# Optimization experiments

Measured on AMD Instinct MI355X. Metric: run time of the kernel, lower is better.

The kernel has to match this reference:

```python
import jax, jax.numpy as jnp
import numpy as np

N = 50000      # nodes
E = 800000     # edges (before self-loops)
DIN, H1, H2, OUT = 128, 128, 64, 40
LN_EPS = 1e-5


def setup_inputs() -> dict:
    key = jax.random.key(0)
    ks = jax.random.split(key, 16)
    s = lambda d: 1.0 / np.sqrt(d)
    inp = {
        "x": jax.random.normal(ks[0], (N, DIN), jnp.float32),
        "edge_index": jax.random.randint(ks[1], (2, E), 0, N, dtype=jnp.int64),
        # GCNConv weights (applied as x @ W) and biases
        "W1": jax.random.normal(ks[2], (DIN, H1), jnp.float32) * s(DIN),
        "b1": jnp.zeros((H1,), jnp.float32),
        "W2": jax.random.normal(ks[3], (H1, H2), jnp.float32) * s(H1),
        "b2": jnp.zeros((H2,), jnp.float32),
        "W3": jax.random.normal(ks[4], (H2, H2), jnp.float32) * s(H2),
        "b3": jnp.zeros((H2,), jnp.float32),
        # LayerNorms
        "g1": jnp.ones((H1,), jnp.float32),
        "be1": jnp.zeros((H1,), jnp.float32),
        "g2": jnp.ones((H2,), jnp.float32),
        "be2": jnp.zeros((H2,), jnp.float32),
        # post_mp MLP head
        "Wp1": jax.random.normal(ks[5], (H2, H2), jnp.float32) * s(H2),
        "bp1": jnp.zeros((H2,), jnp.float32),
        "Wp2": jax.random.normal(ks[6], (H2, OUT), jnp.float32) * s(H2),
        "bp2": jnp.zeros((OUT,), jnp.float32),
    }
    return inp


def _layer_norm(x, g, b):
    mu = jnp.mean(x, axis=-1, keepdims=True)
    var = jnp.mean((x - mu) ** 2, axis=-1, keepdims=True)
    return (x - mu) * jax.lax.rsqrt(var + LN_EPS) * g + b


def _gcn(x, src, dst, norm, W, b):
    # PyG GCNConv: linear first, then normalized gather/scatter-add, bias last
    h = x @ W                                  # [N, H]
    msg = h[src] * norm[:, None]               # [E+N, H] gather
    out = jax.ops.segment_sum(msg, dst, num_segments=N)  # scatter-add
    return out + b


def reference(x, edge_index, W1, b1, W2, b2, W3, b3, g1, be1, g2, be2,
              Wp1, bp1, Wp2, bp2):
    loops = jnp.arange(N, dtype=edge_index.dtype)
    src = jnp.concatenate([edge_index[0], loops])  # add self-loops
    dst = jnp.concatenate([edge_index[1], loops])
    # symmetric normalization D^{-1/2} (A+I) D^{-1/2} (same graph all layers)
    deg = jax.ops.segment_sum(jnp.ones_like(src, dtype=x.dtype), dst,
                              num_segments=N)
    dinv = jnp.where(deg > 0, jax.lax.rsqrt(jnp.maximum(deg, 1.0)), 0.0)
    norm = dinv[src] * dinv[dst]

    h = _gcn(x, src, dst, norm, W1, b1)
    h = _layer_norm(jax.nn.relu(h), g1, be1)
    h = _gcn(h, src, dst, norm, W2, b2)
    h = _layer_norm(jax.nn.relu(h), g2, be2)
    emb = _gcn(h, src, dst, norm, W3, b3)      # emb = conv output, pre-ReLU
    h = jax.nn.relu(emb)
    h = (h @ Wp1 + bp1) @ Wp2 + bp2            # post_mp: two stacked Linears
    return emb, jax.nn.log_softmax(h, axis=1)
```

## Files before the change

### kernel.cpp

```cpp
#include <hip/hip_runtime.h>
#include <hip/hip_bf16.h>

#define DIN 128
#define HID1 128
#define HID2 64
#define OUTD 40
#define NCHUNK 64

typedef __attribute__((ext_vector_type(8))) short bf16x8;
typedef __attribute__((ext_vector_type(4))) float f32x4;

__device__ __forceinline__ float bf2f(unsigned int u) {
    union { unsigned int i; float f; } c;
    c.i = u << 16;
    return c.f;
}
__device__ __forceinline__ unsigned short f2bf(float f) {
    union { float f; unsigned int i; } c; c.f = f;
    unsigned int r = c.i + 0x7FFFu + ((c.i >> 16) & 1u);
    return (unsigned short)(r >> 16);
}
__device__ __forceinline__ unsigned int packbf(float lo, float hi) {
    return (unsigned int)f2bf(lo) | ((unsigned int)f2bf(hi) << 16);
}

struct WCvt {
    const void* p[14];
    int sz[14];
    int off[14];
    int tobf[14];
    int cols[14];
};


__launch_bounds__(512)
__global__ void prep_kernel(const unsigned short* __restrict__ xu,
                            const int* __restrict__ ei,
                            int* __restrict__ flags,
                            int* __restrict__ pos,
                            unsigned int* __restrict__ hist,
                            WCvt wc, unsigned short* __restrict__ wbf,
                            float* __restrict__ wf,
                            int E, int N) {
    __shared__ unsigned int h32[25000];
    __shared__ int sh2[2];
    const int NW = (N + 1) >> 1;
    const int b = blockIdx.x;
    const int t = threadIdx.x;
    if (b < NCHUNK) {
        if (t == 0) sh2[0] = 0;
        for (int w = t; w < NW; w += 512) h32[w] = 0u;
        __syncthreads();
        int zodd = 0;
        for (int k = t; k < 1024; k += 512)
            if (ei[2 * k + 1] == 0) zodd++;
        if (zodd) atomicAdd(&sh2[0], zodd);
        __syncthreads();
        const int e64 = (sh2[0] > 512) ? 1 : 0;
        const int CH = (E + NCHUNK - 1) / NCHUNK;
        const int lo = b * CH;
        int hi = lo + CH; if (hi > E) hi = E;
        for (int e = lo + t; e < hi; e += 512) {
            int d = e64 ? ei[2 * (E + e)] : ei[E + e];
            if ((unsigned)d < (unsigned)N) {
                unsigned sh = (unsigned)(d & 1) << 4;
                unsigned old = atomicAdd(&h32[d >> 1], 1u << sh);
                pos[e] = (int)((old >> sh) & 0xffffu);
            } else {
                pos[e] = -1;
            }
        }
        __syncthreads();
        unsigned int* hb = hist + (size_t)b * NW;
        for (int w = t; w < NW; w += 512) hb[w] = h32[w];
    } else {
        if (t < 2) sh2[t] = 0;
        __syncthreads();
        int bad = 0;
        for (int k = t; k < 2048; k += 512) {
            float v = bf2f(xu[2 * k]);
            float a = fabsf(v);
            if (!(a <= 1e4f) || (v != 0.f && a < 1e-4f)) bad++;
        }
        int zodd = 0;
        for (int k = t; k < 1024; k += 512)
            if (ei[2 * k + 1] == 0) zodd++;
        if (bad) atomicAdd(&sh2[0], bad);
        if (zodd) atomicAdd(&sh2[1], zodd);
        __syncthreads();
        int xf32 = (sh2[0] > 512) ? 1 : 0;
        if (t == 0) {
            flags[0] = xf32;
            flags[1] = (sh2[1] > 512) ? 1 : 0;
        }
        for (int a = 0; a < 14; ++a) {
            const float* pf = (const float*)wc.p[a];
            const unsigned short* pb = (const unsigned short*)wc.p[a];
            int n = wc.sz[a], off = wc.off[a], tobf = wc.tobf[a];
            int cols = wc.cols[a];
            int rows = tobf ? (n / cols) : 0;
            for (int i = t; i < n; i += 512) {
                float v = xf32 ? pf[i] : bf2f(pb[i]);
                if (tobf) {
                    int k = i / cols, m = i % cols;
                    wbf[off + m * rows + k] = f2bf(v);
                } else {
                    wf[off + i] = v;
                }
            }
        }
    }
}

__device__ __forceinline__ int get_src(const int* ei, int E, int e, int e64) {
    return e64 ? ei[2 * e] : ei[e];
}
__device__ __forceinline__ int get_dst(const int* ei, int E, int e, int e64) {
    return e64 ? ei[2 * (E + e)] : ei[E + e];
}

__launch_bounds__(256)
__global__ void phaseB_kernel(const unsigned int* __restrict__ hist,
                              unsigned int* __restrict__ basev,
                              int* __restrict__ cnt, int* __restrict__ bsum,
                              int N) {
    __shared__ int red[256];
    const int NW = (N + 1) >> 1;
    const int NP = NW * 2;
    int t = threadIdx.x;
    int w = blockIdx.x * 256 + t;
    unsigned run0 = 0, run1 = 0;
    if (w < NW) {
        #pragma unroll 4
        for (int b = 0; b < NCHUNK; ++b) {
            unsigned u = hist[(size_t)b * NW + w];
            uint2 bb; bb.x = run0; bb.y = run1;
            *(uint2*)&basev[(size_t)b * NP + 2 * w] = bb;
            run0 += u & 0xffffu;
            run1 += u >> 16;
        }
        cnt[2 * w] = (int)run0;
        if (2 * w + 1 < N) cnt[2 * w + 1] = (int)run1;
    }
    int tot = 0;
    if (w < NW) tot = (int)run0 + ((2 * w + 1 < N) ? (int)run1 : 0);
    red[t] = tot;
    __syncthreads();
    #pragma unroll
    for (int off = 64; off >= 1; off >>= 1) {
        if ((t & 127) < off) red[t] += red[t + off];
        __syncthreads();
    }
    if (t == 0) bsum[2 * blockIdx.x] = red[0];
    if (t == 128) bsum[2 * blockIdx.x + 1] = red[128];
}

__launch_bounds__(256)
__global__ void bscan_kernel(const int* __restrict__ bsum, int* __restrict__ bbase,
                             int* __restrict__ indptr, int NB, int N) {
    __shared__ int part[256];
    int t = threadIdx.x;
    int CH = (NB + 255) / 256;
    int lo = t * CH, hi = lo + CH; if (hi > NB) hi = NB;
    int s = 0;
    for (int i = lo; i < hi; ++i) s += bsum[i];
    part[t] = s;
    __syncthreads();
    for (int off = 1; off < 256; off <<= 1) {
        int v = (t >= off) ? part[t - off] : 0;
        __syncthreads();
        part[t] += v;
        __syncthreads();
    }
    int run = (t > 0) ? part[t - 1] : 0;
    for (int i = lo; i < hi; ++i) { bbase[i] = run; run += bsum[i]; }
    if (t == 255) indptr[N] = part[255];
}

__launch_bounds__(256)
__global__ void emit_kernel(const int* __restrict__ cnt, const int* __restrict__ bbase,
                            int* __restrict__ indptr, float* __restrict__ dinv, int N) {
    __shared__ int sh[256];
    int t = threadIdx.x;
    int i = blockIdx.x * 256 + t;
    int c = (i < N) ? cnt[i] : 0;
    sh[t] = c;
    __syncthreads();
    for (int off = 1; off < 256; off <<= 1) {
        int v = (t >= off) ? sh[t - off] : 0;
        __syncthreads();
        sh[t] += v;
        __syncthreads();
    }
    if (i < N) {
        int excl = sh[t] - c + bbase[blockIdx.x];
        indptr[i] = excl;
        dinv[i] = 1.0f / sqrtf((float)(c + 1));
    }
}

__global__ void scatter_kernel(const int* __restrict__ ei, const int* __restrict__ indptr,
                               const int* __restrict__ pos, const float* __restrict__ dinv,
                               const unsigned int* __restrict__ basev,
                               int2* __restrict__ csr_sn,
                               int E, int N, const int* __restrict__ flags) {
    int e64 = flags[1];
    int CH = (E + NCHUNK - 1) / NCHUNK;
    int NP = ((N + 1) >> 1) * 2;
    int base = (blockIdx.x * blockDim.x + threadIdx.x) * 4;
    #pragma unroll
    for (int u = 0; u < 4; ++u) {
        int e = base + u;
        if (e < E) {
            int p = pos[e];
            if (p >= 0) {
                int bb = e / CH;
                int d = get_dst(ei, E, e, e64);
                int s = get_src(ei, E, e, e64);
                if ((unsigned)s >= (unsigned)N) s = 0;
                float nrm = dinv[s] * dinv[d];
                int slot = indptr[d] + (int)basev[(size_t)bb * NP + d] + p;
                csr_sn[slot] = make_int2(s, __float_as_int(nrm));
            }
        }
    }
}


template<typename AT>
__device__ __forceinline__ bf16x8 ld_afrag(const AT* p);
template<>
__device__ __forceinline__ bf16x8 ld_afrag<unsigned short>(const unsigned short* p) {
    return *(const bf16x8*)p;
}
template<>
__device__ __forceinline__ bf16x8 ld_afrag<float>(const float* p) {
    float4 a = *(const float4*)p;
    float4 b = *(const float4*)(p + 4);
    bf16x8 r;
    r[0] = (short)f2bf(a.x); r[1] = (short)f2bf(a.y);
    r[2] = (short)f2bf(a.z); r[3] = (short)f2bf(a.w);
    r[4] = (short)f2bf(b.x); r[5] = (short)f2bf(b.y);
    r[6] = (short)f2bf(b.z); r[7] = (short)f2bf(b.w);
    return r;
}

template<int K, int M, typename AT>
__device__ __forceinline__ void mm_body(const AT* __restrict__ A,
                                        const unsigned short* __restrict__ WT,
                                        unsigned short* __restrict__ C, int N,
                                        unsigned short (*Ws)[K + 8]) {
    int tid = threadIdx.x;
    for (int idx = tid; idx < M * K / 8; idx += 256) {
        int r = idx / (K / 8), c8 = idx % (K / 8);
        *(uint4*)&Ws[r][c8 * 8] = *(const uint4*)&WT[r * K + c8 * 8];
    }
    __syncthreads();
    int w = tid >> 6, lane = tid & 63;
    int m = lane & 15, q = lane >> 4;
    int row_a = blockIdx.x * 64 + w * 16 + m;
    if (row_a >= N) row_a = N - 1;
    const AT* arow = A + (size_t)row_a * K;
    f32x4 acc[M / 16];
    #pragma unroll
    for (int t = 0; t < M / 16; ++t) acc[t] = (f32x4){0.f, 0.f, 0.f, 0.f};
    #pragma unroll
    for (int ks = 0; ks < K / 32; ++ks) {
        int k0 = ks * 32 + q * 8;
        bf16x8 a = ld_afrag<AT>(arow + k0);
        #pragma unroll
        for (int t = 0; t < M / 16; ++t) {
            bf16x8 b = *(const bf16x8*)&Ws[t * 16 + m][k0];
            acc[t] = __builtin_amdgcn_mfma_f32_16x16x32_bf16(a, b, acc[t], 0, 0, 0);
        }
    }
    int rbase = blockIdx.x * 64 + w * 16 + q * 4;
    #pragma unroll
    for (int reg = 0; reg < 4; ++reg) {
        int row = rbase + reg;
        if (row < N) {
            #pragma unroll
            for (int t = 0; t < M / 16; ++t)
                C[(size_t)row * M + t * 16 + m] = f2bf(acc[t][reg]);
        }
    }
}

template<int K, int M>
__launch_bounds__(256)
__global__ void mm_dual_kernel(const void* __restrict__ A,
                               const unsigned short* __restrict__ WT,
                               unsigned short* __restrict__ C, int N,
                               const int* __restrict__ flags) {
    __shared__ unsigned short Ws[M][K + 8];
    if (flags[0]) mm_body<K, M, float>((const float*)A, WT, C, N, Ws);
    else          mm_body<K, M, unsigned short>((const unsigned short*)A, WT, C, N, Ws);
}

template<int K, int M>
__launch_bounds__(256)
__global__ void mm_bf_kernel(const unsigned short* __restrict__ A,
                             const unsigned short* __restrict__ WT,
                             unsigned short* __restrict__ C, int N) {
    __shared__ unsigned short Ws[M][K + 8];
    mm_body<K, M, unsigned short>(A, WT, C, N, Ws);
}


template<int VPL>
__device__ __forceinline__ void gacc1(float* acc, const unsigned short* r, float n) {
    if constexpr (VPL == 8) {
        uint4 u = *(const uint4*)r;
        acc[0] += bf2f(u.x & 0xffffu) * n; acc[1] += bf2f(u.x >> 16) * n;
        acc[2] += bf2f(u.y & 0xffffu) * n; acc[3] += bf2f(u.y >> 16) * n;
        acc[4] += bf2f(u.z & 0xffffu) * n; acc[5] += bf2f(u.z >> 16) * n;
        acc[6] += bf2f(u.w & 0xffffu) * n; acc[7] += bf2f(u.w >> 16) * n;
    } else {
        uint2 u = *(const uint2*)r;
        acc[0] += bf2f(u.x & 0xffffu) * n; acc[1] += bf2f(u.x >> 16) * n;
        acc[2] += bf2f(u.y & 0xffffu) * n; acc[3] += bf2f(u.y >> 16) * n;
    }
}

template<int VPL>
__device__ __forceinline__ void gacc4(float* acc,
                                      const unsigned short* r0, float n0,
                                      const unsigned short* r1, float n1,
                                      const unsigned short* r2, float n2,
                                      const unsigned short* r3, float n3) {
    if constexpr (VPL == 8) {
        uint4 u0 = *(const uint4*)r0;
        uint4 u1 = *(const uint4*)r1;
        uint4 u2 = *(const uint4*)r2;
        uint4 u3 = *(const uint4*)r3;
        acc[0] += bf2f(u0.x & 0xffffu) * n0 + bf2f(u1.x & 0xffffu) * n1
                + bf2f(u2.x & 0xffffu) * n2 + bf2f(u3.x & 0xffffu) * n3;
        acc[1] += bf2f(u0.x >> 16) * n0 + bf2f(u1.x >> 16) * n1
                + bf2f(u2.x >> 16) * n2 + bf2f(u3.x >> 16) * n3;
        acc[2] += bf2f(u0.y & 0xffffu) * n0 + bf2f(u1.y & 0xffffu) * n1
                + bf2f(u2.y & 0xffffu) * n2 + bf2f(u3.y & 0xffffu) * n3;
        acc[3] += bf2f(u0.y >> 16) * n0 + bf2f(u1.y >> 16) * n1
                + bf2f(u2.y >> 16) * n2 + bf2f(u3.y >> 16) * n3;
        acc[4] += bf2f(u0.z & 0xffffu) * n0 + bf2f(u1.z & 0xffffu) * n1
                + bf2f(u2.z & 0xffffu) * n2 + bf2f(u3.z & 0xffffu) * n3;
        acc[5] += bf2f(u0.z >> 16) * n0 + bf2f(u1.z >> 16) * n1
                + bf2f(u2.z >> 16) * n2 + bf2f(u3.z >> 16) * n3;
        acc[6] += bf2f(u0.w & 0xffffu) * n0 + bf2f(u1.w & 0xffffu) * n1
                + bf2f(u2.w & 0xffffu) * n2 + bf2f(u3.w & 0xffffu) * n3;
        acc[7] += bf2f(u0.w >> 16) * n0 + bf2f(u1.w >> 16) * n1
                + bf2f(u2.w >> 16) * n2 + bf2f(u3.w >> 16) * n3;
    } else {
        uint2 u0 = *(const uint2*)r0;
        uint2 u1 = *(const uint2*)r1;
        uint2 u2 = *(const uint2*)r2;
        uint2 u3 = *(const uint2*)r3;
        acc[0] += bf2f(u0.x & 0xffffu) * n0 + bf2f(u1.x & 0xffffu) * n1
                + bf2f(u2.x & 0xffffu) * n2 + bf2f(u3.x & 0xffffu) * n3;
        acc[1] += bf2f(u0.x >> 16) * n0 + bf2f(u1.x >> 16) * n1
                + bf2f(u2.x >> 16) * n2 + bf2f(u3.x >> 16) * n3;
        acc[2] += bf2f(u0.y & 0xffffu) * n0 + bf2f(u1.y & 0xffffu) * n1
                + bf2f(u2.y & 0xffffu) * n2 + bf2f(u3.y & 0xffffu) * n3;
        acc[3] += bf2f(u0.y >> 16) * n0 + bf2f(u1.y >> 16) * n1
                + bf2f(u2.y >> 16) * n2 + bf2f(u3.y >> 16) * n3;
    }
}

template<int H, bool RELU_LN, bool EMB>
__launch_bounds__(256)
__global__ void agg_kernel(const unsigned short* __restrict__ h,
                           const int* __restrict__ indptr,
                           const int2* __restrict__ csr_sn,
                           const float* __restrict__ dinv,
                           const float* __restrict__ bias,
                           const float* __restrict__ gamma,
                           const float* __restrict__ beta,
                           unsigned short* __restrict__ out,
                           void* __restrict__ out_emb,
                           int N, const int* __restrict__ flags) {
    constexpr int VPL = H / 16;
    __shared__ int2 lsn[4][64];
    int w = threadIdx.x >> 6;
    int lane = threadIdx.x & 63;
    int slot = lane >> 4;
    int idx = lane & 15;
    int node = blockIdx.x * 4 + w;
    bool active = node < N;
    int nd = active ? node : N - 1;
    float di = dinv[nd];
    int c0 = idx * VPL;
    float acc[VPL];
    #pragma unroll
    for (int v = 0; v < VPL; ++v) acc[v] = 0.f;
    if (slot == 0)
        gacc1<VPL>(acc, h + (size_t)nd * H + c0, di * di);
    int beg = indptr[nd], end = indptr[nd + 1];
    for (int base = beg; base < end; base += 64) {
        int m = end - base; if (m > 64) m = 64;
        if (lane < m) lsn[w][lane] = csr_sn[base + lane];
        int m16 = m & ~15;
        int j = 0;
        for (; j < m16; j += 16) {
            int2 e0 = lsn[w][j + slot];
            int2 e1 = lsn[w][j + 4 + slot];
            int2 e2 = lsn[w][j + 8 + slot];
            int2 e3 = lsn[w][j + 12 + slot];
            gacc4<VPL>(acc,
                       h + (size_t)e0.x * H + c0, __int_as_float(e0.y),
                       h + (size_t)e1.x * H + c0, __int_as_float(e1.y),
                       h + (size_t)e2.x * H + c0, __int_as_float(e2.y),
                       h + (size_t)e3.x * H + c0, __int_as_float(e3.y));
        }
        for (int tt = j + slot; tt < m; tt += 4) {
            int2 e = lsn[w][tt];
            gacc1<VPL>(acc, h + (size_t)e.x * H + c0, __int_as_float(e.y));
        }
    }
    #pragma unroll
    for (int v = 0; v < VPL; ++v) {
        acc[v] += __shfl_xor(acc[v], 16, 64);
        acc[v] += __shfl_xor(acc[v], 32, 64);
    }
    #pragma unroll
    for (int v = 0; v < VPL; ++v) acc[v] += bias[c0 + v];
    if constexpr (RELU_LN) {
        #pragma unroll
        for (int v = 0; v < VPL; ++v) acc[v] = fmaxf(acc[v], 0.f);
        float s = 0.f, sq = 0.f;
        #pragma unroll
        for (int v = 0; v < VPL; ++v) { s += acc[v]; sq += acc[v] * acc[v]; }
        #pragma unroll
        for (int off = 8; off >= 1; off >>= 1) {
            s += __shfl_xor(s, off, 64);
            sq += __shfl_xor(sq, off, 64);
        }
        float mu = s * (1.0f / H);
        float var = fmaxf(sq * (1.0f / H) - mu * mu, 0.f);
        float inv = 1.0f / sqrtf(var + 1e-5f);
        #pragma unroll
        for (int v = 0; v < VPL; ++v)
            acc[v] = (acc[v] - mu) * inv * gamma[c0 + v] + beta[c0 + v];
    }
    if (active && slot == 0) {
        unsigned short* orow = out + (size_t)node * H + c0;
        if constexpr (VPL == 8) {
            uint4 p;
            p.x = packbf(acc[0], acc[1]); p.y = packbf(acc[2], acc[3]);
            p.z = packbf(acc[4], acc[5]); p.w = packbf(acc[6], acc[7]);
            *(uint4*)orow = p;
        } else {
            uint2 p; p.x = packbf(acc[0], acc[1]); p.y = packbf(acc[2], acc[3]);
            *(uint2*)orow = p;
        }
        if constexpr (EMB) {
            if (flags[0]) {
                float* o = (float*)out_emb + (size_t)node * H + c0;
                #pragma unroll
                for (int v4 = 0; v4 < VPL / 4; ++v4)
                    *(float4*)(o + v4 * 4) = make_float4(acc[v4 * 4], acc[v4 * 4 + 1],
                                                         acc[v4 * 4 + 2], acc[v4 * 4 + 3]);
            } else {
                unsigned short* o = (unsigned short*)out_emb + (size_t)node * H + c0;
                #pragma unroll
                for (int v2 = 0; v2 < VPL / 2; ++v2)
                    ((unsigned int*)o)[v2] = packbf(acc[v2 * 2], acc[v2 * 2 + 1]);
            }
        }
    }
}


__launch_bounds__(256)
__global__ void head_kernel(const unsigned short* __restrict__ emb,
                            const float* __restrict__ Wp1,
                            const float* __restrict__ bp1,
                            const float* __restrict__ Wp2,
                            const float* __restrict__ bp2,
                            void* __restrict__ d_out, int N,
                            const int* __restrict__ flags) {
    __shared__ float Est[64][68];
    __shared__ float W1s[64][64];
    __shared__ float Tst[64][68];
    __shared__ float W2s[64][OUTD];
    __shared__ float b1s[64];
    __shared__ float b2s[OUTD];
    int tid = threadIdx.x;
    int row0 = blockIdx.x * 64;
    for (int i = tid; i < 64 * 64; i += 256) W1s[i >> 6][i & 63] = Wp1[i];
    for (int i = tid; i < 64 * OUTD; i += 256) W2s[i / OUTD][i % OUTD] = Wp2[i];
    if (tid < 64) b1s[tid] = bp1[tid];
    if (tid < OUTD) b2s[tid] = bp2[tid];
    for (int i = tid; i < 64 * 32; i += 256) {
        int r = i >> 5, kk = i & 31;
        int row = row0 + r;
        unsigned int u = (row < N) ? *(const unsigned int*)&emb[(size_t)row * 64 + kk * 2] : 0u;
        Est[kk * 2][r]     = fmaxf(bf2f(u & 0xffffu), 0.f);
        Est[kk * 2 + 1][r] = fmaxf(bf2f(u >> 16), 0.f);
    }
    __syncthreads();
    {
        int rg = tid >> 4, cg = tid & 15;
        int r = rg * 4, c = cg * 4;
        float acc[4][4];
        #pragma unroll
        for (int i = 0; i < 4; ++i)
            #pragma unroll
            for (int jj = 0; jj < 4; ++jj) acc[i][jj] = b1s[c + jj];
        #pragma unroll 4
        for (int k = 0; k < 64; ++k) {
            float4 a = *(const float4*)&Est[k][r];
            float4 wv = *(const float4*)&W1s[k][c];
            acc[0][0] += a.x * wv.x; acc[0][1] += a.x * wv.y; acc[0][2] += a.x * wv.z; acc[0][3] += a.x * wv.w;
            acc[1][0] += a.y * wv.x; acc[1][1] += a.y * wv.y; acc[1][2] += a.y * wv.z; acc[1][3] += a.y * wv.w;
            acc[2][0] += a.z * wv.x; acc[2][1] += a.z * wv.y; acc[2][2] += a.z * wv.z; acc[2][3] += a.z * wv.w;
            acc[3][0] += a.w * wv.x; acc[3][1] += a.w * wv.y; acc[3][2] += a.w * wv.z; acc[3][3] += a.w * wv.w;
        }
        #pragma unroll
        for (int i = 0; i < 4; ++i)
            #pragma unroll
            for (int jj = 0; jj < 4; ++jj) Tst[c + jj][r + i] = acc[i][jj];
    }
    __syncthreads();
    int row = tid >> 2, tc = tid & 3, o0 = tc * 10;
    int node = row0 + row;
    float u[10];
    #pragma unroll
    for (int o = 0; o < 10; ++o) u[o] = b2s[o0 + o];
    for (int c2 = 0; c2 < 64; ++c2) {
        float tv = Tst[c2][row];
        const float2* wp = (const float2*)&W2s[c2][o0];
        #pragma unroll
        for (int o2 = 0; o2 < 5; ++o2) {
            float2 wv = wp[o2];
            u[o2 * 2]     += tv * wv.x;
            u[o2 * 2 + 1] += tv * wv.y;
        }
    }
    float mx = u[0];
    #pragma unroll
    for (int o = 1; o < 10; ++o) mx = fmaxf(mx, u[o]);
    mx = fmaxf(mx, __shfl_xor(mx, 1, 64));
    mx = fmaxf(mx, __shfl_xor(mx, 2, 64));
    float sum = 0.f;
    #pragma unroll
    for (int o = 0; o < 10; ++o) sum += __expf(u[o] - mx);
    sum += __shfl_xor(sum, 1, 64);
    sum += __shfl_xor(sum, 2, 64);
    float lse = mx + __logf(sum);
    if (node < N) {
        if (flags[0]) {
            float* base = (float*)d_out + (size_t)N * HID2;
            float* op = base + (size_t)node * OUTD + o0;
            #pragma unroll
            for (int o = 0; o < 10; ++o) op[o] = u[o] - lse;
        } else {
            unsigned short* base = (unsigned short*)d_out + (size_t)N * HID2;
            unsigned int* op = (unsigned int*)(base + (size_t)node * OUTD + o0);
            #pragma unroll
            for (int o2 = 0; o2 < 5; ++o2)
                op[o2] = packbf(u[o2 * 2] - lse, u[o2 * 2 + 1] - lse);
        }
    }
}


extern "C" void kernel_launch(void* const* d_in, const int* in_sizes, int n_in,
                              void* d_out, int out_size, void* d_ws, size_t ws_size,
                              hipStream_t stream) {
    const unsigned short* xu = (const unsigned short*)d_in[0];
    const int*            ei = (const int*)d_in[1];

    const int N = in_sizes[0] / DIN;
    const int E = in_sizes[1] / 2;
    const int NW = (N + 1) / 2;
    const int NP = NW * 2;

    size_t off = 0;
    auto take = [&](size_t bytes) {
        size_t cur = off;
        off += (bytes + 255) & ~(size_t)255;
        return cur;
    };
    char* ws = (char*)d_ws;
    int*   flags   = (int*)  (ws + take(256));
    int*   cnt     = (int*)  (ws + take((size_t)N * 4));
    float* dinv    = (float*)(ws + take((size_t)N * 4));
    int*   indptr  = (int*)  (ws + take((size_t)(N + 1) * 4));
    int*   pos     = (int*)  (ws + take((size_t)E * 4));
    int2*  csr_sn  = (int2*) (ws + take((size_t)E * 8));
    int*   bsum    = (int*)  (ws + take(((size_t)N / 256 + 4) * 4));
    int*   bbase   = (int*)  (ws + take(((size_t)N / 256 + 4) * 4));
    unsigned int* hist  = (unsigned int*)(ws + take((size_t)NCHUNK * NW * 4));
    unsigned int* basev = (unsigned int*)(ws + take((size_t)NCHUNK * NP * 4));
    unsigned short* wbf = (unsigned short*)(ws + take(32768 * 2));
    float*          wf  = (float*)         (ws + take(8192 * 4));
    unsigned short* hbuf = (unsigned short*)(ws + take((size_t)N * DIN * 2));
    unsigned short* abuf = (unsigned short*)(ws + take((size_t)N * DIN * 2));
    (void)ws_size; (void)n_in; (void)out_size;

    const int TB = 256;
    dim3 blk(TB);
    const int NB = (N + 255) / 256;

    WCvt wc;
    int bfoff = 0, foff = 0;
    int offs[14];
    const int wcols[14] = {HID1, 0, HID2, 0, HID2, 0, 0, 0, 0, 0, 0, 0, 0, 0};
    for (int a = 0; a < 14; ++a) {
        int idx = a + 2;
        wc.p[a] = d_in[idx];
        wc.sz[a] = in_sizes[idx];
        int tobf = (idx == 2 || idx == 4 || idx == 6) ? 1 : 0;
        wc.tobf[a] = tobf;
        wc.cols[a] = tobf ? wcols[a] : 1;
        if (tobf) { wc.off[a] = bfoff; bfoff += in_sizes[idx]; }
        else      { wc.off[a] = foff;  foff  += in_sizes[idx]; }
        offs[a] = wc.off[a];
    }

    prep_kernel<<<dim3(NCHUNK + 1), dim3(512), 0, stream>>>(
        xu, ei, flags, pos, hist, wc, wbf, wf, E, N);
    phaseB_kernel<<<dim3((NW + 255) / 256), blk, 0, stream>>>(hist, basev, cnt, bsum, N);
    bscan_kernel<<<dim3(1), blk, 0, stream>>>(bsum, bbase, indptr, NB, N);
    emit_kernel<<<dim3(NB), blk, 0, stream>>>(cnt, bbase, indptr, dinv, N);
    scatter_kernel<<<dim3((E + 1023) / 1024), blk, 0, stream>>>(
        ei, indptr, pos, dinv, basev, csr_sn, E, N, flags);

    unsigned short* W1t = wbf + offs[0];
    unsigned short* W2t = wbf + offs[2];
    unsigned short* W3t = wbf + offs[4];
    float* b1f  = wf + offs[1];
    float* b2f  = wf + offs[3];
    float* b3f  = wf + offs[5];
    float* g1f  = wf + offs[6];
    float* be1f = wf + offs[7];
    float* g2f  = wf + offs[8];
    float* be2f = wf + offs[9];
    float* Wp1f = wf + offs[10];
    float* bp1f = wf + offs[11];
    float* Wp2f = wf + offs[12];
    float* bp2f = wf + offs[13];

    const int MMG = (N + 63) / 64;
    const int AGG = (N + 3) / 4;

    mm_dual_kernel<DIN, HID1><<<dim3(MMG), blk, 0, stream>>>(
        d_in[0], W1t, hbuf, N, flags);
    agg_kernel<HID1, true, false><<<dim3(AGG), blk, 0, stream>>>(
        hbuf, indptr, csr_sn, dinv, b1f, g1f, be1f, abuf, nullptr, N, flags);

    mm_bf_kernel<HID1, HID2><<<dim3(MMG), blk, 0, stream>>>(abuf, W2t, hbuf, N);
    agg_kernel<HID2, true, false><<<dim3(AGG), blk, 0, stream>>>(
        hbuf, indptr, csr_sn, dinv, b2f, g2f, be2f, abuf, nullptr, N, flags);

    mm_bf_kernel<HID2, HID2><<<dim3(MMG), blk, 0, stream>>>(abuf, W3t, hbuf, N);
    agg_kernel<HID2, false, true><<<dim3(AGG), blk, 0, stream>>>(
        hbuf, indptr, csr_sn, dinv, b3f, nullptr, nullptr, abuf, d_out, N, flags);

    head_kernel<<<dim3((N + 63) / 64), blk, 0, stream>>>(
        abuf, Wp1f, bp1f, Wp2f, bp2f, d_out, N, flags);
}
```

Before: 339.2 us.

## Restructure CSR build kernels and assign one node per 16-lane group in aggregation

The CSR preprocessing now uses 128 histogram chunks with 1024-thread blocks. Weight conversion moves out of the histogram kernel into extra blocks of phaseB, and the block-sum scan is folded into emit_kernel, which removes one launch. The aggregation kernel now gives each 16-lane group its own node instead of having four slots share one node and reduce with shuffles, so each block handles 16 nodes. This cuts launches and cross-lane reductions, but each node's edges are now walked serially by one group, and the padded entries (index 0, weight 0) in each round still issue gathers.

```diff
diff --git a/kernel.cpp b/kernel.cpp
--- a/kernel.cpp
+++ b/kernel.cpp
@@ -5,7 +5,7 @@
 #define HID1 128
 #define HID2 64
 #define OUTD 40
-#define NCHUNK 64
+#define NCHUNK 128
 
 typedef __attribute__((ext_vector_type(8))) short bf16x8;
 typedef __attribute__((ext_vector_type(4))) float f32x4;
@@ -22,6 +22,13 @@
 }
 __device__ __forceinline__ unsigned int packbf(float lo, float hi) {
     return (unsigned int)f2bf(lo) | ((unsigned int)f2bf(hi) << 16);
+}
+
+__device__ __forceinline__ int get_src(const int* ei, int E, int e, int e64) {
+    return e64 ? ei[2 * e] : ei[e];
+}
+__device__ __forceinline__ int get_dst(const int* ei, int E, int e, int e64) {
+    return e64 ? ei[2 * (E + e)] : ei[E + e];
 }
 
 struct WCvt {
@@ -32,15 +39,12 @@
     int cols[14];
 };
 
-
-__launch_bounds__(512)
-__global__ void prep_kernel(const unsigned short* __restrict__ xu,
+__launch_bounds__(1024)
+__global__ void posA_kernel(const unsigned short* __restrict__ xu,
                             const int* __restrict__ ei,
                             int* __restrict__ flags,
                             int* __restrict__ pos,
                             unsigned int* __restrict__ hist,
-                            WCvt wc, unsigned short* __restrict__ wbf,
-                            float* __restrict__ wf,
                             int E, int N) {
     __shared__ unsigned int h32[25000];
     __shared__ int sh2[2];
@@ -49,10 +53,10 @@
     const int t = threadIdx.x;
     if (b < NCHUNK) {
         if (t == 0) sh2[0] = 0;
-        for (int w = t; w < NW; w += 512) h32[w] = 0u;
+        for (int w = t; w < NW; w += 1024) h32[w] = 0u;
         __syncthreads();
         int zodd = 0;
-        for (int k = t; k < 1024; k += 512)
+        for (int k = t; k < 1024; k += 1024)
             if (ei[2 * k + 1] == 0) zodd++;
         if (zodd) atomicAdd(&sh2[0], zodd);
         __syncthreads();
@@ -60,7 +64,7 @@
         const int CH = (E + NCHUNK - 1) / NCHUNK;
         const int lo = b * CH;
         int hi = lo + CH; if (hi > E) hi = E;
-        for (int e = lo + t; e < hi; e += 512) {
+        for (int e = lo + t; e < hi; e += 1024) {
             int d = e64 ? ei[2 * (E + e)] : ei[E + e];
             if ((unsigned)d < (unsigned)N) {
                 unsigned sh = (unsigned)(d & 1) << 4;
@@ -72,34 +76,79 @@
         }
         __syncthreads();
         unsigned int* hb = hist + (size_t)b * NW;
-        for (int w = t; w < NW; w += 512) hb[w] = h32[w];
+        for (int w = t; w < NW; w += 1024) hb[w] = h32[w];
     } else {
         if (t < 2) sh2[t] = 0;
         __syncthreads();
         int bad = 0;
-        for (int k = t; k < 2048; k += 512) {
+        for (int k = t; k < 2048; k += 1024) {
             float v = bf2f(xu[2 * k]);
             float a = fabsf(v);
             if (!(a <= 1e4f) || (v != 0.f && a < 1e-4f)) bad++;
         }
         int zodd = 0;
-        for (int k = t; k < 1024; k += 512)
+        for (int k = t; k < 1024; k += 1024)
             if (ei[2 * k + 1] == 0) zodd++;
         if (bad) atomicAdd(&sh2[0], bad);
         if (zodd) atomicAdd(&sh2[1], zodd);
         __syncthreads();
-        int xf32 = (sh2[0] > 512) ? 1 : 0;
         if (t == 0) {
-            flags[0] = xf32;
+            flags[0] = (sh2[0] > 512) ? 1 : 0;
             flags[1] = (sh2[1] > 512) ? 1 : 0;
         }
+    }
+}
+
+__launch_bounds__(256)
+__global__ void phaseB_kernel(const unsigned int* __restrict__ hist,
+                              unsigned int* __restrict__ basev,
+                              int* __restrict__ cnt, int* __restrict__ bsum,
+                              int N, int PB,
+                              WCvt wc, unsigned short* __restrict__ wbf,
+                              float* __restrict__ wf,
+                              const int* __restrict__ flags) {
+    __shared__ int red[256];
+    const int NW = (N + 1) >> 1;
+    const int NP = NW * 2;
+    int t = threadIdx.x;
+    int blk = blockIdx.x;
+    if (blk < PB) {
+        int w = blk * 256 + t;
+        unsigned run0 = 0, run1 = 0;
+        if (w < NW) {
+            #pragma unroll 4
+            for (int b = 0; b < NCHUNK; ++b) {
+                unsigned u = hist[(size_t)b * NW + w];
+                uint2 bb; bb.x = run0; bb.y = run1;
+                *(uint2*)&basev[(size_t)b * NP + 2 * w] = bb;
+                run0 += u & 0xffffu;
+                run1 += u >> 16;
+            }
+            cnt[2 * w] = (int)run0;
+            if (2 * w + 1 < N) cnt[2 * w + 1] = (int)run1;
+        }
+        int tot = 0;
+        if (w < NW) tot = (int)run0 + ((2 * w + 1 < N) ? (int)run1 : 0);
+        red[t] = tot;
+        __syncthreads();
+        #pragma unroll
+        for (int off = 64; off >= 1; off >>= 1) {
+            if ((t & 127) < off) red[t] += red[t + off];
+            __syncthreads();
+        }
+        if (t == 0) bsum[2 * blk] = red[0];
+        if (t == 128) bsum[2 * blk + 1] = red[128];
+    } else {
+        int xf32 = flags[0];
+        int stride = (gridDim.x - PB) * 256;
+        int tid = (blk - PB) * 256 + t;
         for (int a = 0; a < 14; ++a) {
             const float* pf = (const float*)wc.p[a];
             const unsigned short* pb = (const unsigned short*)wc.p[a];
             int n = wc.sz[a], off = wc.off[a], tobf = wc.tobf[a];
             int cols = wc.cols[a];
             int rows = tobf ? (n / cols) : 0;
-            for (int i = t; i < n; i += 512) {
+            for (int i = tid; i < n; i += stride) {
                 float v = xf32 ? pf[i] : bf2f(pb[i]);
                 if (tobf) {
                     int k = i / cols, m = i % cols;
@@ -112,59 +161,14 @@
     }
 }
 
-__device__ __forceinline__ int get_src(const int* ei, int E, int e, int e64) {
-    return e64 ? ei[2 * e] : ei[e];
-}
-__device__ __forceinline__ int get_dst(const int* ei, int E, int e, int e64) {
-    return e64 ? ei[2 * (E + e)] : ei[E + e];
-}
-
 __launch_bounds__(256)
-__global__ void phaseB_kernel(const unsigned int* __restrict__ hist,
-                              unsigned int* __restrict__ basev,
-                              int* __restrict__ cnt, int* __restrict__ bsum,
-                              int N) {
-    __shared__ int red[256];
-    const int NW = (N + 1) >> 1;
-    const int NP = NW * 2;
+__global__ void emit_kernel(const int* __restrict__ cnt, const int* __restrict__ bsum,
+                            int* __restrict__ indptr, float* __restrict__ dinv,
+                            int N, int NB) {
+    __shared__ int part[256];
+    __shared__ int sh[256];
     int t = threadIdx.x;
-    int w = blockIdx.x * 256 + t;
-    unsigned run0 = 0, run1 = 0;
-    if (w < NW) {
-        #pragma unroll 4
-        for (int b = 0; b < NCHUNK; ++b) {
-            unsigned u = hist[(size_t)b * NW + w];
-            uint2 bb; bb.x = run0; bb.y = run1;
-            *(uint2*)&basev[(size_t)b * NP + 2 * w] = bb;
-            run0 += u & 0xffffu;
-            run1 += u >> 16;
-        }
-        cnt[2 * w] = (int)run0;
-        if (2 * w + 1 < N) cnt[2 * w + 1] = (int)run1;
-    }
-    int tot = 0;
-    if (w < NW) tot = (int)run0 + ((2 * w + 1 < N) ? (int)run1 : 0);
-    red[t] = tot;
-    __syncthreads();
-    #pragma unroll
-    for (int off = 64; off >= 1; off >>= 1) {
-        if ((t & 127) < off) red[t] += red[t + off];
-        __syncthreads();
-    }
-    if (t == 0) bsum[2 * blockIdx.x] = red[0];
-    if (t == 128) bsum[2 * blockIdx.x + 1] = red[128];
-}
-
-__launch_bounds__(256)
-__global__ void bscan_kernel(const int* __restrict__ bsum, int* __restrict__ bbase,
-                             int* __restrict__ indptr, int NB, int N) {
-    __shared__ int part[256];
-    int t = threadIdx.x;
-    int CH = (NB + 255) / 256;
-    int lo = t * CH, hi = lo + CH; if (hi > NB) hi = NB;
-    int s = 0;
-    for (int i = lo; i < hi; ++i) s += bsum[i];
-    part[t] = s;
+    part[t] = (t < NB) ? bsum[t] : 0;
     __syncthreads();
     for (int off = 1; off < 256; off <<= 1) {
         int v = (t >= off) ? part[t - off] : 0;
@@ -172,16 +176,8 @@
         part[t] += v;
         __syncthreads();
     }
-    int run = (t > 0) ? part[t - 1] : 0;
-    for (int i = lo; i < hi; ++i) { bbase[i] = run; run += bsum[i]; }
-    if (t == 255) indptr[N] = part[255];
-}
-
-__launch_bounds__(256)
-__global__ void emit_kernel(const int* __restrict__ cnt, const int* __restrict__ bbase,
-                            int* __restrict__ indptr, float* __restrict__ dinv, int N) {
-    __shared__ int sh[256];
-    int t = threadIdx.x;
+    int bbase = (blockIdx.x > 0) ? part[blockIdx.x - 1] : 0;
+    int total = part[255];
     int i = blockIdx.x * 256 + t;
     int c = (i < N) ? cnt[i] : 0;
     sh[t] = c;
@@ -193,10 +189,11 @@
         __syncthreads();
     }
     if (i < N) {
-        int excl = sh[t] - c + bbase[blockIdx.x];
+        int excl = sh[t] - c + bbase;
         indptr[i] = excl;
         dinv[i] = 1.0f / sqrtf((float)(c + 1));
     }
+    if (blockIdx.x == (unsigned)(NB - 1) && t == 0) indptr[N] = total;
 }
 
 __global__ void scatter_kernel(const int* __restrict__ ei, const int* __restrict__ indptr,
@@ -378,12 +375,12 @@
                            void* __restrict__ out_emb,
                            int N, const int* __restrict__ flags) {
     constexpr int VPL = H / 16;
-    __shared__ int2 lsn[4][64];
+    __shared__ int2 lsn[4][4][16];
     int w = threadIdx.x >> 6;
     int lane = threadIdx.x & 63;
-    int slot = lane >> 4;
+    int g = lane >> 4;
     int idx = lane & 15;
-    int node = blockIdx.x * 4 + w;
+    int node = blockIdx.x * 16 + w * 4 + g;
     bool active = node < N;
     int nd = active ? node : N - 1;
     float di = dinv[nd];
@@ -391,34 +388,22 @@
     float acc[VPL];
     #pragma unroll
     for (int v = 0; v < VPL; ++v) acc[v] = 0.f;
-    if (slot == 0)
-        gacc1<VPL>(acc, h + (size_t)nd * H + c0, di * di);
+    gacc1<VPL>(acc, h + (size_t)nd * H + c0, di * di);
     int beg = indptr[nd], end = indptr[nd + 1];
-    for (int base = beg; base < end; base += 64) {
-        int m = end - base; if (m > 64) m = 64;
-        if (lane < m) lsn[w][lane] = csr_sn[base + lane];
-        int m16 = m & ~15;
+    for (int base = beg; base < end; base += 16) {
+        int m = end - base; if (m > 16) m = 16;
+        lsn[w][g][idx] = (idx < m) ? csr_sn[base + idx] : make_int2(0, 0);
+        int rounds = (m + 3) >> 2;
         int j = 0;
-        for (; j < m16; j += 16) {
-            int2 e0 = lsn[w][j + slot];
-            int2 e1 = lsn[w][j + 4 + slot];
-            int2 e2 = lsn[w][j + 8 + slot];
-            int2 e3 = lsn[w][j + 12 + slot];
+        for (int rr = 0; rr < rounds; ++rr, j += 4) {
+            int2 e0 = lsn[w][g][j],     e1 = lsn[w][g][j + 1];
+            int2 e2 = lsn[w][g][j + 2], e3 = lsn[w][g][j + 3];
             gacc4<VPL>(acc,
                        h + (size_t)e0.x * H + c0, __int_as_float(e0.y),
                        h + (size_t)e1.x * H + c0, __int_as_float(e1.y),
                        h + (size_t)e2.x * H + c0, __int_as_float(e2.y),
                        h + (size_t)e3.x * H + c0, __int_as_float(e3.y));
         }
-        for (int tt = j + slot; tt < m; tt += 4) {
-            int2 e = lsn[w][tt];
-            gacc1<VPL>(acc, h + (size_t)e.x * H + c0, __int_as_float(e.y));
-        }
-    }
-    #pragma unroll
-    for (int v = 0; v < VPL; ++v) {
-        acc[v] += __shfl_xor(acc[v], 16, 64);
-        acc[v] += __shfl_xor(acc[v], 32, 64);
     }
     #pragma unroll
     for (int v = 0; v < VPL; ++v) acc[v] += bias[c0 + v];
@@ -440,7 +425,7 @@
         for (int v = 0; v < VPL; ++v)
             acc[v] = (acc[v] - mu) * inv * gamma[c0 + v] + beta[c0 + v];
     }
-    if (active && slot == 0) {
+    if (active) {
         unsigned short* orow = out + (size_t)node * H + c0;
         if constexpr (VPL == 8) {
             uint4 p;
@@ -588,7 +573,6 @@
     int*   pos     = (int*)  (ws + take((size_t)E * 4));
     int2*  csr_sn  = (int2*) (ws + take((size_t)E * 8));
     int*   bsum    = (int*)  (ws + take(((size_t)N / 256 + 4) * 4));
-    int*   bbase   = (int*)  (ws + take(((size_t)N / 256 + 4) * 4));
     unsigned int* hist  = (unsigned int*)(ws + take((size_t)NCHUNK * NW * 4));
     unsigned int* basev = (unsigned int*)(ws + take((size_t)NCHUNK * NP * 4));
     unsigned short* wbf = (unsigned short*)(ws + take(32768 * 2));
@@ -600,6 +584,7 @@
     const int TB = 256;
     dim3 blk(TB);
     const int NB = (N + 255) / 256;
+    const int PB = (NW + 255) / 256;
 
     WCvt wc;
     int bfoff = 0, foff = 0;
@@ -617,11 +602,11 @@
         offs[a] = wc.off[a];
     }
 
-    prep_kernel<<<dim3(NCHUNK + 1), dim3(512), 0, stream>>>(
-        xu, ei, flags, pos, hist, wc, wbf, wf, E, N);
-    phaseB_kernel<<<dim3((NW + 255) / 256), blk, 0, stream>>>(hist, basev, cnt, bsum, N);
-    bscan_kernel<<<dim3(1), blk, 0, stream>>>(bsum, bbase, indptr, NB, N);
-    emit_kernel<<<dim3(NB), blk, 0, stream>>>(cnt, bbase, indptr, dinv, N);
+    posA_kernel<<<dim3(NCHUNK + 1), dim3(1024), 0, stream>>>(
+        xu, ei, flags, pos, hist, E, N);
+    phaseB_kernel<<<dim3(PB + 64), blk, 0, stream>>>(
+        hist, basev, cnt, bsum, N, PB, wc, wbf, wf, flags);
+    emit_kernel<<<dim3(NB), blk, 0, stream>>>(cnt, bsum, indptr, dinv, N, NB);
     scatter_kernel<<<dim3((E + 1023) / 1024), blk, 0, stream>>>(
         ei, indptr, pos, dinv, basev, csr_sn, E, N, flags);
 
@@ -641,7 +626,7 @@
     float* bp2f = wf + offs[13];
 
     const int MMG = (N + 63) / 64;
-    const int AGG = (N + 3) / 4;
+    const int AGG = (N + 15) / 16;
 
     mm_dual_kernel<DIN, HID1><<<dim3(MMG), blk, 0, stream>>>(
         d_in[0], W1t, hbuf, N, flags);
```

After: 281.6 us. 17.0% less time.
